# Kernel tuning notes

Hardware: AMD Instinct MI355X
Metric: run time of the kernel (lower is better)

Reference implementation:

```python
import jax, jax.numpy as jnp
import numpy as np

EPS = 1e-4


def setup_inputs() -> dict:
    key = jax.random.key(0)
    k1, k2, k3 = jax.random.split(key, 3)
    B, C, H, W = 8, 3, 1024, 1024
    n_axis, n_knots = 8, 16
    raw = jax.random.uniform(k1, (B, C, H, W), dtype=jnp.float32)
    ys = jax.random.uniform(k2, (B, n_axis, n_knots), dtype=jnp.float32)
    A = jax.random.normal(k3, (B, C, n_axis), dtype=jnp.float32)
    return {"raw": raw, "ys": ys, "A": A}


def reference(raw, ys, A):
    # raw: [B,3,H,W], ys: [B,n_axis,K], A: [B,3,n_axis]
    B, C, H, W = raw.shape
    K = ys.shape[-1]
    pinv_A = jnp.linalg.pinv(A)                      # [B, n_axis, 3]
    mins = jnp.sum(A * (A < 0), axis=1)              # [B, n_axis]
    maxs = jnp.sum(A * (A > 0), axis=1)              # [B, n_axis]

    # project pixels onto axes: [B, n_axis, H, W]
    f = jnp.einsum('bchw,bca->bahw', raw, A)

    # knot x-positions (uniform per batch/axis): [B, n_axis, K+2]
    t = jnp.linspace(0.0, 1.0, K + 2, dtype=raw.dtype)[None, None]
    xs = t * (maxs + EPS - mins)[..., None] + mins[..., None]
    ys_full = jnp.concatenate([mins[..., None], ys, maxs[..., None]], axis=-1)  # [B,A,K+2]
    dx = xs[..., 1] - xs[..., 0]                     # [B, n_axis]
    slopes = jnp.diff(ys_full, axis=-1) / dx[..., None]  # [B, n_axis, K+1]

    # segment index per pixel (replaces masked loop): floor((f - xs0)/dx)
    idx = jnp.clip(jnp.floor((f - mins[..., None, None]) / dx[..., None, None]),
                   0, K).astype(jnp.int32)           # [B, n_axis, H, W]

    idx_flat = idx.reshape(B, -1, H * W)             # [B, n_axis, HW]
    ys_hi = jnp.take_along_axis(ys_full, idx_flat + 1, axis=-1).reshape(f.shape)
    xs_hi = jnp.take_along_axis(xs, idx_flat + 1, axis=-1).reshape(f.shape)
    sl = jnp.take_along_axis(slopes, idx_flat, axis=-1).reshape(f.shape)

    est = ys_hi - (xs_hi - f) * sl                   # [B, n_axis, H, W]

    # project back to RGB: [B, 3, H, W]
    out = jnp.einsum('bahw,bac->bchw', est, pinv_A)
    return out
```

## Files before the change

### kernel.cpp

```cpp
#include <hip/hip_runtime.h>
#include <hip/hip_bf16.h>

#define EPS 1e-4f
#define NAXIS 8
#define NKNOTS 16
#define NSEG 17
#define WS_STRIDE 384
#define TBL_N 336

__global__ void spline_prep(const float* __restrict__ ys,
                            const float* __restrict__ A,
                            float* __restrict__ ws) {
    const int b = blockIdx.x;
    const float* Ab  = A  + (size_t)b * 3 * NAXIS;
    const float* ysb = ys + (size_t)b * NAXIS * NKNOTS;
    float* w = ws + (size_t)b * WS_STRIDE;
    __shared__ double Ginv[9];
    const int tid = threadIdx.x;

    if (tid == 0) {
        double G[9];
        for (int i = 0; i < 3; ++i)
            for (int j = 0; j < 3; ++j) {
                double s = 0.0;
                for (int a = 0; a < NAXIS; ++a)
                    s += (double)Ab[i * NAXIS + a] * (double)Ab[j * NAXIS + a];
                G[i * 3 + j] = s;
            }
        const double g00 = G[0], g01 = G[1], g02 = G[2];
        const double g11 = G[4], g12 = G[5], g22 = G[8];
        const double det = g00 * (g11 * g22 - g12 * g12)
                         - g01 * (g01 * g22 - g12 * g02)
                         + g02 * (g01 * g12 - g11 * g02);
        const double inv = 1.0 / det;
        Ginv[0] = (g11 * g22 - g12 * g12) * inv;
        Ginv[1] = (g02 * g12 - g01 * g22) * inv;
        Ginv[2] = (g01 * g12 - g02 * g11) * inv;
        Ginv[3] = Ginv[1];
        Ginv[4] = (g00 * g22 - g02 * g02) * inv;
        Ginv[5] = (g02 * g01 - g00 * g12) * inv;
        Ginv[6] = Ginv[2];
        Ginv[7] = Ginv[5];
        Ginv[8] = (g00 * g11 - g01 * g01) * inv;
    }
    __syncthreads();

    if (tid < 24) {
        const int a = tid / 3, c = tid % 3;
        double s = 0.0;
        for (int i = 0; i < 3; ++i)
            s += (double)Ab[i * NAXIS + a] * Ginv[i * 3 + c];
        w[a * 3 + c]      = (float)s;
        w[24 + a * 3 + c] = Ab[c * NAXIS + a];
    }
    if (tid < NAXIS) {
        const int a = tid;
        float mn = 0.f, mx = 0.f;
        for (int c = 0; c < 3; ++c) {
            const float v = Ab[c * NAXIS + a];
            mn += (v < 0.f) ? v : 0.f;
            mx += (v > 0.f) ? v : 0.f;
        }
        const float range = mx + EPS - mn;
        const float dx = range / 17.0f;
        w[48 + a] = mn;
        w[56 + a] = 1.0f / dx;
        float yf[NKNOTS + 2];
        yf[0] = mn;
        for (int k = 0; k < NKNOTS; ++k) yf[k + 1] = ysb[a * NKNOTS + k];
        yf[NKNOTS + 1] = mx;
        for (int s = 0; s < NSEG; ++s) {
            const float sl  = (yf[s + 1] - yf[s]) / dx;
            const float xhi = ((float)(s + 1) / 17.0f) * range + mn;
            w[64 + (a * NSEG + s) * 2 + 0] = sl;
            w[64 + (a * NSEG + s) * 2 + 1] = yf[s + 1] - xhi * sl;
        }
    }
}

__global__ __launch_bounds__(256) void spline_main(const float* __restrict__ raw,
                                                   const float* __restrict__ ws,
                                                   float* __restrict__ out,
                                                   int blocksPerBatch, int HW) {
    const int b    = blockIdx.x / blocksPerBatch;
    const int tile = blockIdx.x % blocksPerBatch;

    __shared__ float s[TBL_N];
    {
        const float* w = ws + (size_t)b * WS_STRIDE;
        for (int i = threadIdx.x; i < TBL_N; i += 256) s[i] = w[i];
    }
    __syncthreads();

    const float*  sp   = s;
    const float*  sA   = s + 24;
    const float*  smn  = s + 48;
    const float*  sid  = s + 56;
    const float2* sseg = (const float2*)(s + 64);

    const size_t base = (size_t)b * 3 * HW + (size_t)tile * 1024 + threadIdx.x * 4;
    const float4 r4 = *(const float4*)(raw + base);
    const float4 g4 = *(const float4*)(raw + base + HW);
    const float4 b4 = *(const float4*)(raw + base + 2 * (size_t)HW);

    float4 o0, o1, o2;
    float* o0p = &o0.x; float* o1p = &o1.x; float* o2p = &o2.x;
    const float* rp = &r4.x; const float* gp = &g4.x; const float* bp = &b4.x;

    #pragma unroll
    for (int p = 0; p < 4; ++p) {
        const float rc = rp[p], gc = gp[p], bc = bp[p];
        float a0 = 0.f, a1 = 0.f, a2 = 0.f;
        #pragma unroll
        for (int a = 0; a < NAXIS; ++a) {
            const float fa = fmaf(rc, sA[a * 3 + 0],
                             fmaf(gc, sA[a * 3 + 1], bc * sA[a * 3 + 2]));
            int idx = (int)floorf((fa - smn[a]) * sid[a]);
            idx = idx < 0 ? 0 : (idx > NKNOTS ? NKNOTS : idx);
            const float2 ci = sseg[a * NSEG + idx];
            const float est = fmaf(ci.x, fa, ci.y);
            a0 = fmaf(est, sp[a * 3 + 0], a0);
            a1 = fmaf(est, sp[a * 3 + 1], a1);
            a2 = fmaf(est, sp[a * 3 + 2], a2);
        }
        o0p[p] = a0; o1p[p] = a1; o2p[p] = a2;
    }

    *(float4*)(out + base)                  = o0;
    *(float4*)(out + base + HW)             = o1;
    *(float4*)(out + base + 2 * (size_t)HW) = o2;
}

extern "C" void kernel_launch(void* const* d_in, const int* in_sizes, int n_in,
                              void* d_out, int out_size, void* d_ws, size_t ws_size,
                              hipStream_t stream) {
    const float* raw = (const float*)d_in[0];
    const float* ys  = (const float*)d_in[1];
    const float* A   = (const float*)d_in[2];
    float* out = (float*)d_out;
    float* ws  = (float*)d_ws;

    const int B  = in_sizes[2] / (3 * NAXIS);
    const int HW = in_sizes[0] / (B * 3);
    const int blocksPerBatch = HW / 1024;

    spline_prep<<<B, 64, 0, stream>>>(ys, A, ws);
    spline_main<<<B * blocksPerBatch, 256, 0, stream>>>(raw, ws, out, blocksPerBatch, HW);
}
```

Before: 185.6 us.

## Process multiple tiles per block with register prefetch and nontemporal stores

```diff
diff --git a/kernel.cpp b/kernel.cpp
--- a/kernel.cpp
+++ b/kernel.cpp
@@ -5,8 +5,10 @@
 #define NAXIS 8
 #define NKNOTS 16
 #define NSEG 17
+#define GRP 8
 #define WS_STRIDE 384
-#define TBL_N 336
+
+typedef float vf4 __attribute__((ext_vector_type(4)));
 
 __global__ void spline_prep(const float* __restrict__ ys,
                             const float* __restrict__ A,
@@ -63,14 +65,15 @@
         }
         const float range = mx + EPS - mn;
         const float dx = range / 17.0f;
-        w[48 + a] = mn;
-        w[56 + a] = 1.0f / dx;
+        const float invdx = 1.0f / dx;
+        w[48 + a] = -mn * invdx;
+        w[56 + a] = invdx;
         float yf[NKNOTS + 2];
         yf[0] = mn;
         for (int k = 0; k < NKNOTS; ++k) yf[k + 1] = ysb[a * NKNOTS + k];
         yf[NKNOTS + 1] = mx;
         for (int s = 0; s < NSEG; ++s) {
-            const float sl  = (yf[s + 1] - yf[s]) / dx;
+            const float sl  = (yf[s + 1] - yf[s]) * invdx;
             const float xhi = ((float)(s + 1) / 17.0f) * range + mn;
             w[64 + (a * NSEG + s) * 2 + 0] = sl;
             w[64 + (a * NSEG + s) * 2 + 1] = yf[s + 1] - xhi * sl;
@@ -78,57 +81,64 @@
     }
 }
 
-__global__ __launch_bounds__(256) void spline_main(const float* __restrict__ raw,
-                                                   const float* __restrict__ ws,
-                                                   float* __restrict__ out,
-                                                   int blocksPerBatch, int HW) {
+__global__ __launch_bounds__(256, 4) void spline_main(const float* __restrict__ raw,
+                                                      const float* __restrict__ ws,
+                                                      float* __restrict__ out,
+                                                      int blocksPerBatch, int HW) {
     const int b    = blockIdx.x / blocksPerBatch;
     const int tile = blockIdx.x % blocksPerBatch;
+    const float* w = ws + (size_t)b * WS_STRIDE;
 
-    __shared__ float s[TBL_N];
-    {
-        const float* w = ws + (size_t)b * WS_STRIDE;
-        for (int i = threadIdx.x; i < TBL_N; i += 256) s[i] = w[i];
-    }
+    __shared__ float2 sseg[NAXIS * NSEG];
+    for (int i = threadIdx.x; i < NAXIS * NSEG; i += 256)
+        sseg[i] = ((const float2*)(w + 64))[i];
     __syncthreads();
 
-    const float*  sp   = s;
-    const float*  sA   = s + 24;
-    const float*  smn  = s + 48;
-    const float*  sid  = s + 56;
-    const float2* sseg = (const float2*)(s + 64);
+    const size_t pb = (size_t)b * 3 * HW;
+    const int px0 = tile * (1024 * GRP) + threadIdx.x * 4;
 
-    const size_t base = (size_t)b * 3 * HW + (size_t)tile * 1024 + threadIdx.x * 4;
-    const float4 r4 = *(const float4*)(raw + base);
-    const float4 g4 = *(const float4*)(raw + base + HW);
-    const float4 b4 = *(const float4*)(raw + base + 2 * (size_t)HW);
-
-    float4 o0, o1, o2;
-    float* o0p = &o0.x; float* o1p = &o1.x; float* o2p = &o2.x;
-    const float* rp = &r4.x; const float* gp = &g4.x; const float* bp = &b4.x;
+    vf4 cr = *(const vf4*)(raw + pb + px0);
+    vf4 cg = *(const vf4*)(raw + pb + HW + px0);
+    vf4 cb = *(const vf4*)(raw + pb + 2 * (size_t)HW + px0);
 
     #pragma unroll
-    for (int p = 0; p < 4; ++p) {
-        const float rc = rp[p], gc = gp[p], bc = bp[p];
-        float a0 = 0.f, a1 = 0.f, a2 = 0.f;
+    for (int g = 0; g < GRP; ++g) {
+        vf4 nr, ng, nb;
+        if (g + 1 < GRP) {
+            const int px = px0 + (g + 1) * 1024;
+            nr = *(const vf4*)(raw + pb + px);
+            ng = *(const vf4*)(raw + pb + HW + px);
+            nb = *(const vf4*)(raw + pb + 2 * (size_t)HW + px);
+        }
+
+        vf4 o0, o1, o2;
         #pragma unroll
-        for (int a = 0; a < NAXIS; ++a) {
-            const float fa = fmaf(rc, sA[a * 3 + 0],
-                             fmaf(gc, sA[a * 3 + 1], bc * sA[a * 3 + 2]));
-            int idx = (int)floorf((fa - smn[a]) * sid[a]);
-            idx = idx < 0 ? 0 : (idx > NKNOTS ? NKNOTS : idx);
-            const float2 ci = sseg[a * NSEG + idx];
-            const float est = fmaf(ci.x, fa, ci.y);
-            a0 = fmaf(est, sp[a * 3 + 0], a0);
-            a1 = fmaf(est, sp[a * 3 + 1], a1);
-            a2 = fmaf(est, sp[a * 3 + 2], a2);
+        for (int p = 0; p < 4; ++p) {
+            const float rc = cr[p], gc = cg[p], bc = cb[p];
+            float a0 = 0.f, a1 = 0.f, a2 = 0.f;
+            #pragma unroll
+            for (int a = 0; a < NAXIS; ++a) {
+                const float fa = fmaf(rc, w[24 + a * 3 + 0],
+                                 fmaf(gc, w[24 + a * 3 + 1], bc * w[24 + a * 3 + 2]));
+                const float t = fmaf(fa, w[56 + a], w[48 + a]);
+                int idx = (int)t;
+                idx = idx > NKNOTS ? NKNOTS : idx;
+                const float2 ci = sseg[a * NSEG + idx];
+                const float est = fmaf(ci.x, fa, ci.y);
+                a0 = fmaf(est, w[a * 3 + 0], a0);
+                a1 = fmaf(est, w[a * 3 + 1], a1);
+                a2 = fmaf(est, w[a * 3 + 2], a2);
+            }
+            o0[p] = a0; o1[p] = a1; o2[p] = a2;
         }
-        o0p[p] = a0; o1p[p] = a1; o2p[p] = a2;
+
+        const int px = px0 + g * 1024;
+        __builtin_nontemporal_store(o0, (vf4*)(out + pb + px));
+        __builtin_nontemporal_store(o1, (vf4*)(out + pb + HW + px));
+        __builtin_nontemporal_store(o2, (vf4*)(out + pb + 2 * (size_t)HW + px));
+
+        cr = nr; cg = ng; cb = nb;
     }
-
-    *(float4*)(out + base)                  = o0;
-    *(float4*)(out + base + HW)             = o1;
-    *(float4*)(out + base + 2 * (size_t)HW) = o2;
 }
 
 extern "C" void kernel_launch(void* const* d_in, const int* in_sizes, int n_in,
@@ -142,7 +152,7 @@
 
     const int B  = in_sizes[2] / (3 * NAXIS);
     const int HW = in_sizes[0] / (B * 3);
-    const int blocksPerBatch = HW / 1024;
+    const int blocksPerBatch = HW / (1024 * GRP);
 
     spline_prep<<<B, 64, 0, stream>>>(ys, A, ws);
     spline_main<<<B * blocksPerBatch, 256, 0, stream>>>(raw, ws, out, blocksPerBatch, HW);
```

Result: no change. 188.0 us (+1.3%).
